# Optimization experiments

Hardware: AMD Instinct MI355X
Metric: run time of the kernel (lower is better)

## Reference

```python
import jax, jax.numpy as jnp
import numpy as np

SEQ = 2048
D_MODEL = 2048
N_HEAD = 16
D_QK = 128
D_V = 128


def setup_inputs() -> dict:
    key = jax.random.key(0)
    ks = jax.random.split(key, 5)
    return {
        "x": jax.random.normal(ks[0], (SEQ, D_MODEL), dtype=jnp.float32),
        "q": jax.random.normal(ks[1], (N_HEAD, D_MODEL, D_QK), dtype=jnp.float32),
        "k": jax.random.normal(ks[2], (N_HEAD, D_MODEL, D_QK), dtype=jnp.float32),
        "v": jax.random.normal(ks[3], (N_HEAD, D_MODEL, D_V), dtype=jnp.float32),
        "o": jax.random.normal(ks[4], (N_HEAD, D_V, D_MODEL), dtype=jnp.float32),
        "theta_factor": jnp.asarray(10000.0, dtype=jnp.float32),
    }


def _rope_embed(x, theta_factor, d_qk):
    # x: [n_head, seq, d_qk]; faithful to source: rate is LINEAR in theta_factor
    seq = x.shape[1]
    d_rope = d_qk // 2
    rate = theta_factor * (-jnp.arange(d_rope, dtype=x.dtype) / d_rope)  # [d_rope]
    pos = jnp.arange(seq, dtype=x.dtype)                                 # [seq]
    rot = pos[:, None] * rate[None, :]                                   # [seq, d_rope]
    sin, cos = jnp.sin(rot), jnp.cos(rot)
    x1, x2 = x[..., :d_rope], x[..., d_rope:]
    y = jnp.concatenate([cos * x1 - sin * x2, sin * x1 + cos * x2], axis=-1)
    return y / d_qk ** 0.25  # qk_layer_norm is None path


def reference(x, q, k, v, o, theta_factor):
    seq, d_model = x.shape
    n_head, _, d_qk = q.shape
    d_v = v.shape[2]
    scale = 1.0 / jnp.sqrt(jnp.asarray(n_head * d_v * d_model, dtype=x.dtype))
    # causal mask: (tril - 1) * 1e9, as in source
    mask = (jnp.tril(jnp.ones((seq, seq), dtype=x.dtype)) - 1.0) * 1e9
    # per-head projections (vmapped heads expressed as einsum over h)
    rq = _rope_embed(jnp.einsum('sd,hde->hse', x, q), theta_factor, d_qk)
    rk = _rope_embed(jnp.einsum('sd,hde->hse', x, k), theta_factor, d_qk)
    vs = jnp.einsum('sd,hdv->hsv', x, v)
    scores = jnp.einsum('hse,hte->hst', rq, rk) + mask  # [h, s, s]
    w = jax.nn.softmax(scores, axis=-1)
    y = jnp.einsum('hst,htv->hsv', w, vs)
    z = jnp.einsum('hsv,hvd->sd', y, o)
    return z * scale
```

## Files before the change

### kernel.cpp

```cpp
#include <hip/hip_runtime.h>
#include <math.h>


typedef _Float16 half_t;
typedef __attribute__((ext_vector_type(8))) _Float16 half8;
typedef __attribute__((ext_vector_type(4))) float f32x4;

#define SEQ   2048
#define DM    2048
#define NHEAD 16

__device__ __forceinline__ f32x4 mfma16(half8 a, half8 b, f32x4 c) {
  return __builtin_amdgcn_mfma_f32_16x16x32_f16(a, b, c, 0, 0, 0);
}

__device__ __forceinline__ void gll16(const half_t* g, half_t* l) {
  __builtin_amdgcn_global_load_lds(
      (const __attribute__((address_space(1))) unsigned int*)g,
      (__attribute__((address_space(3))) unsigned int*)l, 16, 0, 0);
}

template <int CTRL>
__device__ __forceinline__ float dppf(float v) {
  int r = __builtin_amdgcn_mov_dpp(__builtin_bit_cast(int, v), CTRL, 0xF, 0xF,
                                   true);
  return __builtin_bit_cast(float, r);
}
__device__ __forceinline__ float red16_max(float v) {
  v = fmaxf(v, dppf<0xB1>(v));
  v = fmaxf(v, dppf<0x4E>(v));
  v = fmaxf(v, dppf<0x141>(v));
  v = fmaxf(v, dppf<0x140>(v));
  return v;
}
__device__ __forceinline__ float red16_sum(float v) {
  v += dppf<0xB1>(v);
  v += dppf<0x4E>(v);
  v += dppf<0x141>(v);
  v += dppf<0x140>(v);
  return v;
}

__device__ __forceinline__ void tpose32(const float* __restrict__ in,
                                        half_t* __restrict__ hi,
                                        half_t* __restrict__ lo, int R, int C,
                                        int r0, int c0, float (*tile)[33],
                                        int tid) {
  int tx = tid & 31, ty = tid >> 5;
#pragma unroll
  for (int i = 0; i < 32; i += 8)
    tile[ty + i][tx] = in[(size_t)(r0 + ty + i) * C + c0 + tx];
  __syncthreads();
#pragma unroll
  for (int i = 0; i < 32; i += 8) {
    float v = tile[tx][ty + i];
    half_t h = (half_t)v;
    size_t oidx = (size_t)(c0 + ty + i) * R + r0 + tx;
    hi[oidx] = h;
    if (lo) lo[oidx] = (half_t)(v - (float)h);
  }
}

__global__ __launch_bounds__(256)
void k_pre(const float* __restrict__ x, const float* __restrict__ q,
           const float* __restrict__ k, const float* __restrict__ v,
           const float* __restrict__ o, const float* __restrict__ thetap,
           half_t* __restrict__ Xh, half_t* __restrict__ Xl,
           half_t* __restrict__ WTh, half_t* __restrict__ WTl,
           half_t* __restrict__ VhT, half_t* __restrict__ OT,
           float2* __restrict__ trig) {
  __shared__ float tile[32][33];
  int b = blockIdx.x, tid = threadIdx.x;
  if (b < 4096) {
    int i = b * 256 + tid;
    float4 vv = ((const float4*)x)[i];
    union { half_t h[4]; uint2 u; } H, L;
    H.h[0] = (half_t)vv.x; H.h[1] = (half_t)vv.y;
    H.h[2] = (half_t)vv.z; H.h[3] = (half_t)vv.w;
    L.h[0] = (half_t)(vv.x - (float)H.h[0]);
    L.h[1] = (half_t)(vv.y - (float)H.h[1]);
    L.h[2] = (half_t)(vv.z - (float)H.h[2]);
    L.h[3] = (half_t)(vv.w - (float)H.h[3]);
    *(uint2*)&Xh[(size_t)i * 4] = H.u;
    *(uint2*)&Xl[(size_t)i * 4] = L.u;
  } else if (b < 16384) {
    int j = b - 4096;
    int which = j >> 12, z = (j >> 8) & 15, tb = j & 255;
    int c0 = (tb & 3) * 32, r0 = (tb >> 2) * 32;
    const float* src =
        (which == 0 ? q : which == 1 ? k : v) + (size_t)z * 2048 * 128;
    size_t doff = (size_t)z * 128 * 2048;
    if (which == 0)
      tpose32(src, WTh + doff, WTl + doff, 2048, 128, r0, c0, tile, tid);
    else if (which == 1) {
      size_t koff = (size_t)16 * 128 * 2048 + doff;
      tpose32(src, WTh + koff, WTl + koff, 2048, 128, r0, c0, tile, tid);
    } else
      tpose32(src, VhT + doff, nullptr, 2048, 128, r0, c0, tile, tid);
  } else if (b < 20480) {
    int j = b - 16384;
    int c0 = (j & 63) * 32, r0 = (j >> 6) * 32;
    tpose32(o, OT, nullptr, 2048, 2048, r0, c0, tile, tid);
  } else {
    int idx = (b - 20480) * 256 + tid;
    int s = idx >> 6, e = idx & 63;
    float th = thetap[0];
    float rate = th * (-(float)e * (1.0f / 64.0f));
    float rot = (float)s * rate;
    double rev = (double)rot * 0.15915494309189535;
    double fr = rev - rint(rev);
    float thr = (float)(fr * 6.283185307179586);
    float sn = sinf(thr), cs = cosf(thr);
    const float inv4 = 0.2973017787506803f;
    trig[idx] = make_float2(cs * inv4, sn * inv4);
  }
}

__global__ __launch_bounds__(256, 2)
void k_proj(const half_t* __restrict__ Xh, const half_t* __restrict__ Xl,
            const half_t* __restrict__ WTh, const half_t* __restrict__ WTl,
            const float2* __restrict__ trig, half_t* __restrict__ Rh,
            half_t* __restrict__ Rl) {
  __shared__ __align__(16) char smem[65536];
  half_t* sAh = (half_t*)smem;
  half_t* sAl = (half_t*)(smem + 16384);
  half_t* sBh = (half_t*)(smem + 32768);
  half_t* sBl = (half_t*)(smem + 49152);
  int y = blockIdx.y;
  int m0 = blockIdx.x * 128;
  const half_t* wth = WTh + (size_t)y * 128 * DM;
  const half_t* wtl = WTl + (size_t)y * 128 * DM;
  int lane = threadIdx.x & 63, wave = threadIdx.x >> 6;
  int l15 = lane & 15, quad = lane >> 4;
  int wm = wave >> 1, wn = wave & 1;

  f32x4 acc[4][4];
#pragma unroll
  for (int a = 0; a < 4; ++a)
#pragma unroll
    for (int b = 0; b < 4; ++b) acc[a][b] = (f32x4)0.0f;

  for (int kt = 0; kt < DM / 64; ++kt) {
    int k0 = kt * 64;
#pragma unroll
    for (int i = 0; i < 4; ++i) {
      int c = wave * 4 + i;
      int g = c * 64 + lane;
      int row = g >> 3;
      int lc = (g & 7) ^ (row & 7);
      size_t ro = (size_t)row * DM + k0 + lc * 8;
      gll16(Xh + (size_t)m0 * DM + ro, sAh + c * 512);
      gll16(Xl + (size_t)m0 * DM + ro, sAl + c * 512);
      gll16(wth + ro, sBh + c * 512);
      gll16(wtl + ro, sBl + c * 512);
    }
    __syncthreads();
#pragma unroll
    for (int kk = 0; kk < 2; ++kk) {
      half8 ah[4], al[4], bh[4], bl[4];
#pragma unroll
      for (int t = 0; t < 4; ++t) {
        int ar = wm * 64 + t * 16 + l15;
        int br = wn * 64 + t * 16 + l15;
        int ao = ar * 64 + (((kk * 4 + quad) ^ (ar & 7)) * 8);
        int bo = br * 64 + (((kk * 4 + quad) ^ (br & 7)) * 8);
        ah[t] = *(const half8*)&sAh[ao];
        al[t] = *(const half8*)&sAl[ao];
        bh[t] = *(const half8*)&sBh[bo];
        bl[t] = *(const half8*)&sBl[bo];
      }
#pragma unroll
      for (int im = 0; im < 4; ++im)
#pragma unroll
        for (int in = 0; in < 4; ++in) {
          acc[im][in] = mfma16(ah[im], bh[in], acc[im][in]);
          acc[im][in] = mfma16(ah[im], bl[in], acc[im][in]);
          acc[im][in] = mfma16(al[im], bh[in], acc[im][in]);
        }
    }
    __syncthreads();
  }
  float* tile = (float*)smem;
  size_t ybase = (size_t)y * SEQ * 128;
#pragma unroll
  for (int p = 0; p < 2; ++p) {
    if (p) __syncthreads();
    if (wm == p) {
#pragma unroll
      for (int im = 0; im < 4; ++im)
#pragma unroll
        for (int in = 0; in < 4; ++in)
#pragma unroll
          for (int r = 0; r < 4; ++r)
            tile[(im * 16 + quad * 4 + r) * 132 + wn * 64 + in * 16 + l15] =
                acc[im][in][r];
    }
    __syncthreads();
    int e = lane;
#pragma unroll 4
    for (int rr = 0; rr < 16; ++rr) {
      int rloc = wave * 16 + rr;
      int s = m0 + p * 64 + rloc;
      float x1 = tile[rloc * 132 + e];
      float x2 = tile[rloc * 132 + 64 + e];
      float2 sc = trig[s * 64 + e];
      float y1 = sc.x * x1 - sc.y * x2;
      float y2 = sc.y * x1 + sc.x * x2;
      half_t h1 = (half_t)y1, h2 = (half_t)y2;
      size_t base = ybase + (size_t)s * 128;
      Rh[base + e] = h1;       Rl[base + e] = (half_t)(y1 - (float)h1);
      Rh[base + 64 + e] = h2;  Rl[base + 64 + e] = (half_t)(y2 - (float)h2);
    }
  }
}

template <int HALF_OUT>
__global__ __launch_bounds__(256)
void k_gemm1(const half_t* __restrict__ A, const half_t* __restrict__ B,
             void* __restrict__ Cv, float scale) {
  __shared__ __align__(16) half_t sA[64 * 64], sB[128 * 64];
  int am0 = blockIdx.y * 64, bn0 = blockIdx.x * 128;
  int lane = threadIdx.x & 63, wave = threadIdx.x >> 6;
  int l15 = lane & 15, quad = lane >> 4;
  int wm = wave >> 1, wn = wave & 1;

  f32x4 acc[2][4];
#pragma unroll
  for (int a = 0; a < 2; ++a)
#pragma unroll
    for (int b = 0; b < 4; ++b) acc[a][b] = (f32x4)0.0f;

  for (int kt = 0; kt < DM / 64; ++kt) {
    int k0 = kt * 64;
#pragma unroll
    for (int i = 0; i < 2; ++i) {
      int g0 = (i * 4 + wave) * 64;
      int g = g0 + lane;
      int row = g >> 3;
      int lc = (g & 7) ^ (row & 7);
      gll16(A + (size_t)(am0 + row) * 2048 + k0 + lc * 8, sA + g0 * 8);
    }
#pragma unroll
    for (int i = 0; i < 4; ++i) {
      int g0 = (i * 4 + wave) * 64;
      int g = g0 + lane;
      int row = g >> 3;
      int lc = (g & 7) ^ (row & 7);
      gll16(B + (size_t)(bn0 + row) * 2048 + k0 + lc * 8, sB + g0 * 8);
    }
    __syncthreads();
#pragma unroll
    for (int kk = 0; kk < 2; ++kk) {
      half8 ah[2], bh[4];
#pragma unroll
      for (int t = 0; t < 2; ++t) {
        int ar = wm * 32 + t * 16 + l15;
        ah[t] = *(const half8*)&sA[ar * 64 + (((kk * 4 + quad) ^ (ar & 7)) * 8)];
      }
#pragma unroll
      for (int t = 0; t < 4; ++t) {
        int br = wn * 64 + t * 16 + l15;
        bh[t] = *(const half8*)&sB[br * 64 + (((kk * 4 + quad) ^ (br & 7)) * 8)];
      }
#pragma unroll
      for (int im = 0; im < 2; ++im)
#pragma unroll
        for (int in = 0; in < 4; ++in)
          acc[im][in] = mfma16(ah[im], bh[in], acc[im][in]);
    }
    __syncthreads();
  }
#pragma unroll
  for (int im = 0; im < 2; ++im)
#pragma unroll
    for (int in = 0; in < 4; ++in)
#pragma unroll
      for (int r = 0; r < 4; ++r) {
        int row = am0 + wm * 32 + im * 16 + quad * 4 + r;
        int col = bn0 + wn * 64 + in * 16 + l15;
        if (HALF_OUT)
          ((half_t*)Cv)[(size_t)row * 2048 + col] = (half_t)(acc[im][in][r] * scale);
        else
          ((float*)Cv)[(size_t)row * 2048 + col] = acc[im][in][r] * scale;
      }
}

__global__ __launch_bounds__(256, 2)
void k_flash(const half_t* __restrict__ Rh, const half_t* __restrict__ Rl,
             const half_t* __restrict__ VST, half_t* __restrict__ Ybig) {
  int idx = blockIdx.x;
  int h = idx & 15;
  int qt = (idx < 256) ? (31 - (idx >> 4)) : ((idx - 256) >> 4);
  int lane = threadIdx.x & 63, wave = threadIdx.x >> 6;
  int l15 = lane & 15, quad = lane >> 4;

  const half_t* RQh = Rh + (size_t)h * SEQ * 128;
  const half_t* RQl = Rl + (size_t)h * SEQ * 128;
  const half_t* RKh = Rh + (size_t)(NHEAD + h) * SEQ * 128;
  const half_t* RKl = Rl + (size_t)(NHEAD + h) * SEQ * 128;
  const half_t* Vt  = VST + (size_t)h * 128 * SEQ;

  __shared__ __align__(16) half_t sKh[64 * 128];
  __shared__ __align__(16) half_t sKl[64 * 128];
  __shared__ __align__(16) half_t sVt[128 * 64];
  __shared__ __align__(16) half_t sP[64 * 72];

  int q0 = qt * 64;

  half8 qh[4], ql[4];
#pragma unroll
  for (int kk = 0; kk < 4; ++kk) {
    size_t ad = (size_t)(q0 + wave * 16 + l15) * 128 + kk * 32 + quad * 8;
    qh[kk] = *(const half8*)&RQh[ad];
    ql[kk] = *(const half8*)&RQl[ad];
  }

  float m_st[4], l_st[4];
  f32x4 oacc[8];
#pragma unroll
  for (int r = 0; r < 4; ++r) { m_st[r] = -INFINITY; l_st[r] = 0.0f; }
#pragma unroll
  for (int iv = 0; iv < 8; ++iv) oacc[iv] = (f32x4)0.0f;

  int nkb = qt + 1;
  for (int kb = 0; kb < nkb; ++kb) {
    int t0 = kb * 64;
#pragma unroll
    for (int i = 0; i < 4; ++i) {
      int c = wave * 4 + i;
      int rk = c * 4 + (lane >> 4);
      int ck = (lane & 15) ^ (rk & 15);
      gll16(RKh + (size_t)(t0 + rk) * 128 + ck * 8, sKh + c * 512);
      gll16(RKl + (size_t)(t0 + rk) * 128 + ck * 8, sKl + c * 512);
      int rv = c * 8 + (lane >> 3);
      int cv = (lane & 7) ^ (rv & 7);
      gll16(Vt + (size_t)rv * SEQ + t0 + cv * 8, sVt + c * 512);
    }
    __syncthreads();

    f32x4 sacc[4];
#pragma unroll
    for (int in = 0; in < 4; ++in) sacc[in] = (f32x4)0.0f;
#pragma unroll
    for (int kk = 0; kk < 4; ++kk)
#pragma unroll
      for (int in = 0; in < 4; ++in) {
        int bo = (in * 16 + l15) * 128 + (((kk * 4 + quad) ^ l15) * 8);
        half8 bh = *(const half8*)&sKh[bo];
        half8 bl = *(const half8*)&sKl[bo];
        sacc[in] = mfma16(qh[kk], bh, sacc[in]);
        sacc[in] = mfma16(qh[kk], bl, sacc[in]);
        sacc[in] = mfma16(ql[kk], bh, sacc[in]);
      }
    if (kb == qt) {
#pragma unroll
      for (int in = 0; in < 4; ++in)
#pragma unroll
        for (int r = 0; r < 4; ++r)
          if (in * 16 + l15 > wave * 16 + quad * 4 + r) sacc[in][r] = -1e30f;
    }
    float alpha[4];
#pragma unroll
    for (int r = 0; r < 4; ++r) {
      float mx = fmaxf(fmaxf(sacc[0][r], sacc[1][r]),
                       fmaxf(sacc[2][r], sacc[3][r]));
      mx = red16_max(mx);
      float mnew = fmaxf(m_st[r], mx);
      alpha[r] = __expf(m_st[r] - mnew);
      float sum = 0.0f;
#pragma unroll
      for (int in = 0; in < 4; ++in) {
        float p = __expf(sacc[in][r] - mnew);
        sacc[in][r] = p;
        sum += p;
      }
      sum = red16_sum(sum);
      l_st[r] = l_st[r] * alpha[r] + sum;
      m_st[r] = mnew;
    }
#pragma unroll
    for (int in = 0; in < 4; ++in)
#pragma unroll
      for (int r = 0; r < 4; ++r)
        sP[(wave * 16 + quad * 4 + r) * 72 + in * 16 + l15] =
            (half_t)sacc[in][r];
#pragma unroll
    for (int iv = 0; iv < 8; ++iv)
#pragma unroll
      for (int r = 0; r < 4; ++r) oacc[iv][r] *= alpha[r];

#pragma unroll
    for (int kk2 = 0; kk2 < 2; ++kk2) {
      half8 pa =
          *(const half8*)&sP[(wave * 16 + l15) * 72 + kk2 * 32 + quad * 8];
#pragma unroll
      for (int iv = 0; iv < 8; ++iv) {
        half8 vb = *(const half8*)&sVt[(iv * 16 + l15) * 64 +
                                       (((kk2 * 4 + quad) ^ (l15 & 7)) * 8)];
        oacc[iv] = mfma16(pa, vb, oacc[iv]);
      }
    }
    __syncthreads();
  }
  float invl[4];
#pragma unroll
  for (int r = 0; r < 4; ++r) invl[r] = 1.0f / l_st[r];
#pragma unroll
  for (int iv = 0; iv < 8; ++iv)
#pragma unroll
    for (int r = 0; r < 4; ++r) {
      int row = q0 + wave * 16 + quad * 4 + r;
      int col = h * 128 + iv * 16 + l15;
      Ybig[(size_t)row * 2048 + col] = (half_t)(oacc[iv][r] * invl[r]);
    }
}

extern "C" void kernel_launch(void* const* d_in, const int* in_sizes, int n_in,
                              void* d_out, int out_size, void* d_ws,
                              size_t ws_size, hipStream_t stream) {
  const float* x = (const float*)d_in[0];
  const float* q = (const float*)d_in[1];
  const float* k = (const float*)d_in[2];
  const float* v = (const float*)d_in[3];
  const float* o = (const float*)d_in[4];
  const float* theta = (const float*)d_in[5];
  float* out = (float*)d_out;

  char* ws = (char*)d_ws;
  const size_t HB = (size_t)2048 * 2048 * 2;
  half_t* Xh   = (half_t*)(ws);
  half_t* Xl   = (half_t*)(ws + HB);
  half_t* WTh  = (half_t*)(ws + 2 * HB);
  half_t* WTl  = (half_t*)(ws + 4 * HB);
  half_t* VhT  = (half_t*)(ws + 6 * HB);
  half_t* OT   = (half_t*)(ws + 7 * HB);
  half_t* Rh   = (half_t*)(ws + 8 * HB);
  half_t* Rl   = (half_t*)(ws + 10 * HB);
  float2* trig = (float2*)(ws + 12 * HB);
  half_t* VST  = (half_t*)(ws + 2 * HB);
  half_t* Ybig = (half_t*)(ws + 3 * HB);

  k_pre<<<20992, 256, 0, stream>>>(x, q, k, v, o, theta, Xh, Xl, WTh, WTl,
                                   VhT, OT, trig);
  k_proj<<<dim3(16, 32), 256, 0, stream>>>(Xh, Xl, WTh, WTl, trig, Rh, Rl);
  k_gemm1<1><<<dim3(16, 32), 256, 0, stream>>>(VhT, Xh, VST, 1.0f);
  k_flash<<<512, 256, 0, stream>>>(Rh, Rl, VST, Ybig);
  k_gemm1<0><<<dim3(16, 32), 256, 0, stream>>>(Ybig, OT, out, 1.0f / 2048.0f);
}
```

Measured before the change: 354.7 us.

## Use 128-row query tiles with split-KV halves and a merge kernel

The flash kernel now processes 128 query rows per block, with each wave owning two 16-row subtiles. This halves how often K and V tiles are loaded into LDS per query row. The key range for each query tile is split into two halves handled by separate blocks, which keeps the grid at 512 balanced blocks. Each block writes unnormalized fp32 partial outputs plus its row max and row sum, and a new merge kernel combines the two halves into the fp16 Y buffer. The cost is extra fp32 partial traffic, one more kernel launch, and higher register use per wave.

```diff
diff --git a/kernel.cpp b/kernel.cpp
--- a/kernel.cpp
+++ b/kernel.cpp
@@ -287,10 +287,15 @@
 
 __global__ __launch_bounds__(256, 2)
 void k_flash(const half_t* __restrict__ Rh, const half_t* __restrict__ Rl,
-             const half_t* __restrict__ VST, half_t* __restrict__ Ybig) {
+             const half_t* __restrict__ VST, float* __restrict__ Op0,
+             float* __restrict__ Op1, float* __restrict__ ml) {
   int idx = blockIdx.x;
   int h = idx & 15;
-  int qt = (idx < 256) ? (31 - (idx >> 4)) : ((idx - 256) >> 4);
+  int khalf = idx < 256 ? 0 : 1;
+  int qt = khalf ? ((idx - 256) >> 4) : (15 - (idx >> 4));
+  int hq = h * 16 + qt;
+  int kb0 = khalf ? (qt + 1) : 0;
+  int kb1 = khalf ? (2 * qt + 2) : (qt + 1);
   int lane = threadIdx.x & 63, wave = threadIdx.x >> 6;
   int l15 = lane & 15, quad = lane >> 4;
 
@@ -303,27 +308,33 @@
   __shared__ __align__(16) half_t sKh[64 * 128];
   __shared__ __align__(16) half_t sKl[64 * 128];
   __shared__ __align__(16) half_t sVt[128 * 64];
-  __shared__ __align__(16) half_t sP[64 * 72];
-
-  int q0 = qt * 64;
-
-  half8 qh[4], ql[4];
-#pragma unroll
-  for (int kk = 0; kk < 4; ++kk) {
-    size_t ad = (size_t)(q0 + wave * 16 + l15) * 128 + kk * 32 + quad * 8;
-    qh[kk] = *(const half8*)&RQh[ad];
-    ql[kk] = *(const half8*)&RQl[ad];
-  }
-
-  float m_st[4], l_st[4];
-  f32x4 oacc[8];
-#pragma unroll
-  for (int r = 0; r < 4; ++r) { m_st[r] = -INFINITY; l_st[r] = 0.0f; }
-#pragma unroll
-  for (int iv = 0; iv < 8; ++iv) oacc[iv] = (f32x4)0.0f;
-
-  int nkb = qt + 1;
-  for (int kb = 0; kb < nkb; ++kb) {
+  __shared__ __align__(16) half_t sP[128 * 72];
+
+  int q0 = qt * 128;
+
+  half8 qh[2][4], ql[2][4];
+#pragma unroll
+  for (int im = 0; im < 2; ++im)
+#pragma unroll
+    for (int kk = 0; kk < 4; ++kk) {
+      size_t ad =
+          (size_t)(q0 + wave * 32 + im * 16 + l15) * 128 + kk * 32 + quad * 8;
+      qh[im][kk] = *(const half8*)&RQh[ad];
+      ql[im][kk] = *(const half8*)&RQl[ad];
+    }
+
+  float m_st[2][4], l_st[2][4];
+  f32x4 oacc[2][8];
+#pragma unroll
+  for (int im = 0; im < 2; ++im)
+#pragma unroll
+    for (int r = 0; r < 4; ++r) { m_st[im][r] = -INFINITY; l_st[im][r] = 0.0f; }
+#pragma unroll
+  for (int im = 0; im < 2; ++im)
+#pragma unroll
+    for (int iv = 0; iv < 8; ++iv) oacc[im][iv] = (f32x4)0.0f;
+
+  for (int kb = kb0; kb < kb1; ++kb) {
     int t0 = kb * 64;
 #pragma unroll
     for (int i = 0; i < 4; ++i) {
@@ -338,81 +349,133 @@
     }
     __syncthreads();
 
-    f32x4 sacc[4];
-#pragma unroll
-    for (int in = 0; in < 4; ++in) sacc[in] = (f32x4)0.0f;
-#pragma unroll
-    for (int kk = 0; kk < 4; ++kk)
-#pragma unroll
-      for (int in = 0; in < 4; ++in) {
-        int bo = (in * 16 + l15) * 128 + (((kk * 4 + quad) ^ l15) * 8);
-        half8 bh = *(const half8*)&sKh[bo];
-        half8 bl = *(const half8*)&sKl[bo];
-        sacc[in] = mfma16(qh[kk], bh, sacc[in]);
-        sacc[in] = mfma16(qh[kk], bl, sacc[in]);
-        sacc[in] = mfma16(ql[kk], bh, sacc[in]);
-      }
-    if (kb == qt) {
-#pragma unroll
-      for (int in = 0; in < 4; ++in)
-#pragma unroll
-        for (int r = 0; r < 4; ++r)
-          if (in * 16 + l15 > wave * 16 + quad * 4 + r) sacc[in][r] = -1e30f;
-    }
-    float alpha[4];
-#pragma unroll
-    for (int r = 0; r < 4; ++r) {
-      float mx = fmaxf(fmaxf(sacc[0][r], sacc[1][r]),
-                       fmaxf(sacc[2][r], sacc[3][r]));
-      mx = red16_max(mx);
-      float mnew = fmaxf(m_st[r], mx);
-      alpha[r] = __expf(m_st[r] - mnew);
-      float sum = 0.0f;
-#pragma unroll
-      for (int in = 0; in < 4; ++in) {
-        float p = __expf(sacc[in][r] - mnew);
-        sacc[in][r] = p;
-        sum += p;
-      }
-      sum = red16_sum(sum);
-      l_st[r] = l_st[r] * alpha[r] + sum;
-      m_st[r] = mnew;
-    }
-#pragma unroll
-    for (int in = 0; in < 4; ++in)
-#pragma unroll
-      for (int r = 0; r < 4; ++r)
-        sP[(wave * 16 + quad * 4 + r) * 72 + in * 16 + l15] =
-            (half_t)sacc[in][r];
+    bool live = (q0 + wave * 32 + 31 >= t0);
+    if (live) {
+      f32x4 sacc[2][4];
+#pragma unroll
+      for (int im = 0; im < 2; ++im)
+#pragma unroll
+        for (int in = 0; in < 4; ++in) sacc[im][in] = (f32x4)0.0f;
+#pragma unroll
+      for (int kk = 0; kk < 4; ++kk)
+#pragma unroll
+        for (int in = 0; in < 4; ++in) {
+          int bo = (in * 16 + l15) * 128 + (((kk * 4 + quad) ^ l15) * 8);
+          half8 bh = *(const half8*)&sKh[bo];
+          half8 bl = *(const half8*)&sKl[bo];
+          sacc[0][in] = mfma16(qh[0][kk], bh, sacc[0][in]);
+          sacc[0][in] = mfma16(qh[0][kk], bl, sacc[0][in]);
+          sacc[0][in] = mfma16(ql[0][kk], bh, sacc[0][in]);
+          sacc[1][in] = mfma16(qh[1][kk], bh, sacc[1][in]);
+          sacc[1][in] = mfma16(qh[1][kk], bl, sacc[1][in]);
+          sacc[1][in] = mfma16(ql[1][kk], bh, sacc[1][in]);
+        }
+      if (t0 >= q0) {
+#pragma unroll
+        for (int im = 0; im < 2; ++im)
+#pragma unroll
+          for (int in = 0; in < 4; ++in)
+#pragma unroll
+            for (int r = 0; r < 4; ++r) {
+              int sg = q0 + wave * 32 + im * 16 + quad * 4 + r;
+              int tg = t0 + in * 16 + l15;
+              if (tg > sg) sacc[im][in][r] = -1e30f;
+            }
+      }
+      float alpha[2][4];
+#pragma unroll
+      for (int im = 0; im < 2; ++im)
+#pragma unroll
+        for (int r = 0; r < 4; ++r) {
+          float mx = fmaxf(fmaxf(sacc[im][0][r], sacc[im][1][r]),
+                           fmaxf(sacc[im][2][r], sacc[im][3][r]));
+          mx = red16_max(mx);
+          float mnew = fmaxf(m_st[im][r], mx);
+          alpha[im][r] = __expf(m_st[im][r] - mnew);
+          float sum = 0.0f;
+#pragma unroll
+          for (int in = 0; in < 4; ++in) {
+            float p = __expf(sacc[im][in][r] - mnew);
+            sacc[im][in][r] = p;
+            sum += p;
+          }
+          sum = red16_sum(sum);
+          l_st[im][r] = l_st[im][r] * alpha[im][r] + sum;
+          m_st[im][r] = mnew;
+        }
+#pragma unroll
+      for (int im = 0; im < 2; ++im)
+#pragma unroll
+        for (int in = 0; in < 4; ++in)
+#pragma unroll
+          for (int r = 0; r < 4; ++r)
+            sP[(wave * 32 + im * 16 + quad * 4 + r) * 72 + in * 16 + l15] =
+                (half_t)sacc[im][in][r];
+#pragma unroll
+      for (int im = 0; im < 2; ++im)
+#pragma unroll
+        for (int iv = 0; iv < 8; ++iv)
+#pragma unroll
+          for (int r = 0; r < 4; ++r) oacc[im][iv][r] *= alpha[im][r];
+
+#pragma unroll
+      for (int kk2 = 0; kk2 < 2; ++kk2) {
+        half8 pa0 =
+            *(const half8*)&sP[(wave * 32 + l15) * 72 + kk2 * 32 + quad * 8];
+        half8 pa1 = *(const half8*)&sP[(wave * 32 + 16 + l15) * 72 +
+                                       kk2 * 32 + quad * 8];
+#pragma unroll
+        for (int iv = 0; iv < 8; ++iv) {
+          half8 vb = *(const half8*)&sVt[(iv * 16 + l15) * 64 +
+                                         (((kk2 * 4 + quad) ^ (l15 & 7)) * 8)];
+          oacc[0][iv] = mfma16(pa0, vb, oacc[0][iv]);
+          oacc[1][iv] = mfma16(pa1, vb, oacc[1][iv]);
+        }
+      }
+    }
+    __syncthreads();
+  }
+  float* Ob = (khalf ? Op1 : Op0) + (size_t)hq * 16384;
+#pragma unroll
+  for (int im = 0; im < 2; ++im)
 #pragma unroll
     for (int iv = 0; iv < 8; ++iv)
 #pragma unroll
-      for (int r = 0; r < 4; ++r) oacc[iv][r] *= alpha[r];
-
-#pragma unroll
-    for (int kk2 = 0; kk2 < 2; ++kk2) {
-      half8 pa =
-          *(const half8*)&sP[(wave * 16 + l15) * 72 + kk2 * 32 + quad * 8];
-#pragma unroll
-      for (int iv = 0; iv < 8; ++iv) {
-        half8 vb = *(const half8*)&sVt[(iv * 16 + l15) * 64 +
-                                       (((kk2 * 4 + quad) ^ (l15 & 7)) * 8)];
-        oacc[iv] = mfma16(pa, vb, oacc[iv]);
-      }
-    }
-    __syncthreads();
-  }
-  float invl[4];
-#pragma unroll
-  for (int r = 0; r < 4; ++r) invl[r] = 1.0f / l_st[r];
-#pragma unroll
-  for (int iv = 0; iv < 8; ++iv)
-#pragma unroll
-    for (int r = 0; r < 4; ++r) {
-      int row = q0 + wave * 16 + quad * 4 + r;
-      int col = h * 128 + iv * 16 + l15;
-      Ybig[(size_t)row * 2048 + col] = (half_t)(oacc[iv][r] * invl[r]);
-    }
+      for (int r = 0; r < 4; ++r) {
+        int row = wave * 32 + im * 16 + quad * 4 + r;
+        Ob[row * 128 + iv * 16 + l15] = oacc[im][iv][r];
+      }
+  if (l15 == 0) {
+    float* mlw = ml + (size_t)(hq * 2 + khalf) * 256;
+#pragma unroll
+    for (int im = 0; im < 2; ++im)
+#pragma unroll
+      for (int r = 0; r < 4; ++r) {
+        int row = wave * 32 + im * 16 + quad * 4 + r;
+        mlw[row] = m_st[im][r];
+        mlw[128 + row] = l_st[im][r];
+      }
+  }
+}
+
+__global__ __launch_bounds__(256)
+void k_fmerge(const float* __restrict__ Op0, const float* __restrict__ Op1,
+              const float* __restrict__ ml, half_t* __restrict__ Ybig) {
+  int hq = blockIdx.x;
+  int h = hq >> 4, qt = hq & 15;
+  int col = threadIdx.x & 127, rh = threadIdx.x >> 7;
+  const float* O0 = Op0 + (size_t)hq * 16384;
+  const float* O1 = Op1 + (size_t)hq * 16384;
+  const float* mlb = ml + (size_t)hq * 512;
+  for (int r = rh * 64; r < rh * 64 + 64; ++r) {
+    float m0 = mlb[r], l0 = mlb[128 + r];
+    float m1 = mlb[256 + r], l1 = mlb[384 + r];
+    float mm = fmaxf(m0, m1);
+    float w0 = __expf(m0 - mm), w1 = __expf(m1 - mm);
+    float den = w0 * l0 + w1 * l1;
+    float val = (w0 * O0[r * 128 + col] + w1 * O1[r * 128 + col]) / den;
+    Ybig[(size_t)(qt * 128 + r) * 2048 + h * 128 + col] = (half_t)val;
+  }
 }
 
 extern "C" void kernel_launch(void* const* d_in, const int* in_sizes, int n_in,
@@ -439,11 +502,15 @@
   float2* trig = (float2*)(ws + 12 * HB);
   half_t* VST  = (half_t*)(ws + 2 * HB);
   half_t* Ybig = (half_t*)(ws + 3 * HB);
+  float*  Op0  = (float*)(ws);
+  float*  Op1  = (float*)(ws + 4 * HB);
+  float*  mlb  = (float*)(ws + 6 * HB);
 
   k_pre<<<20992, 256, 0, stream>>>(x, q, k, v, o, theta, Xh, Xl, WTh, WTl,
                                    VhT, OT, trig);
   k_proj<<<dim3(16, 32), 256, 0, stream>>>(Xh, Xl, WTh, WTl, trig, Rh, Rl);
   k_gemm1<1><<<dim3(16, 32), 256, 0, stream>>>(VhT, Xh, VST, 1.0f);
-  k_flash<<<512, 256, 0, stream>>>(Rh, Rl, VST, Ybig);
+  k_flash<<<512, 256, 0, stream>>>(Rh, Rl, VST, Op0, Op1, mlb);
+  k_fmerge<<<256, 256, 0, stream>>>(Op0, Op1, mlb, Ybig);
   k_gemm1<0><<<dim3(16, 32), 256, 0, stream>>>(Ybig, OT, out, 1.0f / 2048.0f);
 }
```

Measured after the change: 368.5 us. +3.9%, slower.
